# Performance work log

Hardware: AMD Instinct MI355X
Metric: run time of the kernel (lower is better)

The kernel has to match this reference:

```python
import jax, jax.numpy as jnp
import numpy as np

N_PAIR = 45  # n_agents=10 -> 10*9/2
TINY_THR = np.sqrt(np.finfo(np.float32).tiny).astype(np.float32) * N_PAIR


def setup_inputs() -> dict:
    key = jax.random.key(0)
    ks = jax.random.split(key, 8)
    bs, T, din, H = 4096, 64, 512, 64
    s = lambda fan: 1.0 / np.sqrt(fan)
    return {
        "main": jax.random.normal(ks[0], (1, bs, T, din), jnp.float32),
        "hidden_states": jnp.zeros((1, bs, 1, H), jnp.float32),
        "epsilons": jax.random.uniform(ks[1], (bs, 1), jnp.float32),
        "W_fc1": jax.random.normal(ks[2], (H, din), jnp.float32) * s(din),
        "b_fc1": jnp.zeros((H,), jnp.float32),
        "W_ih": jax.random.normal(ks[3], (3 * H, H), jnp.float32) * s(H),
        "W_hh": jax.random.normal(ks[4], (3 * H, H), jnp.float32) * s(H),
        "b_ih": jnp.zeros((3 * H,), jnp.float32),
        "b_hh": jnp.zeros((3 * H,), jnp.float32),
        "W_out": jax.random.normal(ks[5], (N_PAIR, H), jnp.float32) * s(H),
        "b_out": jnp.zeros((N_PAIR,), jnp.float32),
    }


def reference(main, hidden_states, epsilons, W_fc1, b_fc1, W_ih, W_hh, b_ih, b_hh, W_out, b_out):
    x = main[0]                       # [bs, T, din]
    h0 = hidden_states[0, :, 0, :]    # [bs, H]
    H = h0.shape[-1]

    # Encoder: fc1 + relu (time-independent, fully batched)
    enc = jax.nn.relu(jnp.einsum('bti,oi->bto', x, W_fc1) + b_fc1)  # [bs,T,H]
    # Precompute input-side GRU gates for all timesteps
    gi = jnp.einsum('bth,gh->btg', enc, W_ih) + b_ih                # [bs,T,3H]
    gi_t = jnp.transpose(gi, (1, 0, 2))                             # [T,bs,3H]

    def step(h, g_in):
        gh = h @ W_hh.T + b_hh
        i_r, i_z, i_n = jnp.split(g_in, 3, axis=-1)
        h_r, h_z, h_n = jnp.split(gh, 3, axis=-1)
        r = jax.nn.sigmoid(i_r + h_r)
        z = jax.nn.sigmoid(i_z + h_z)
        n = jnp.tanh(i_n + r * h_n)
        h_new = (1.0 - z) * n + z * h
        return h_new, h_new

    _, hs = jax.lax.scan(step, h0, gi_t)          # hs: [T,bs,H]
    hs = jnp.transpose(hs, (1, 0, 2))             # [bs,T,H]

    # Output head + custom exp-normalize with zero-sum guard
    logits = jnp.einsum('bth,oh->bto', hs, W_out) + b_out  # [bs,T,N_PAIR]
    p = jnp.exp(logits)
    p_sum = jnp.sum(p, axis=-1, keepdims=True)
    p_sum = jnp.where(p_sum <= TINY_THR, 1.0, p_sum)
    p = p / p_sum

    # Epsilon-greedy mixing (softmax exploration, not test_mode)
    eps = epsilons[:, None, :]                    # [bs,1,1]
    p = eps / N_PAIR + p * (1.0 - eps)

    x_out = p[None]                               # [1,bs,T,N_PAIR]
    h_out = hs[None]                              # [1,bs,T,H]
    return (x_out, h_out)
```

## Files before the change

### kernel.cpp

```cpp
#include <hip/hip_runtime.h>

typedef __attribute__((ext_vector_type(4))) float  f32x4;
typedef __attribute__((ext_vector_type(4))) __bf16 bf16x4;
typedef __attribute__((ext_vector_type(8))) __bf16 bf16x8;

#define MFMA16 __builtin_amdgcn_mfma_f32_16x16x32_bf16
#define TINY_THR 4.8789098e-18f
#define XOUT_N ((size_t)4096 * 64 * 45)
#define GI_LD 196

__device__ __forceinline__ void bar_lds() {
  asm volatile("s_waitcnt lgkmcnt(0)\n\ts_barrier" ::: "memory");
}

__device__ __forceinline__ int swz_off(int row, int col) {
  return row * 128 + (((col) << 1) ^ ((row & 7) << 4));
}

__device__ __forceinline__ bf16x8 read_frag(const __bf16* p, int row, int col) {
  const char* base = (const char*)p + row * 128;
  const int r7 = (row & 7) << 4;
  bf16x4 a = *(const bf16x4*)(base + (((col) << 1) ^ r7));
  bf16x4 b = *(const bf16x4*)(base + (((col + 16) << 1) ^ r7));
  bf16x8 r;
  r[0] = a[0]; r[1] = a[1]; r[2] = a[2]; r[3] = a[3];
  r[4] = b[0]; r[5] = b[1]; r[6] = b[2]; r[7] = b[3];
  return r;
}

__device__ __forceinline__ void split_bf16(float v, __bf16& h, __bf16& l) {
  h = (__bf16)v;
  l = (__bf16)(v - (float)h);
}

__global__ void k_prepW(const float* __restrict__ Wfc, __bf16* __restrict__ Wpk) {
  const int idx = blockIdx.x * 256 + threadIdx.x;
  const float v = Wfc[idx];
  __bf16 h, l; split_bf16(v, h, l);
  const int row = idx >> 9, k = idx & 511;
  const int c = k >> 6, col = k & 63;
  Wpk[(c * 2 + 0) * 4096 + row * 64 + col] = h;
  Wpk[(c * 2 + 1) * 4096 + row * 64 + col] = l;
}

__global__ __launch_bounds__(256, 4) void k_encgemm(
    const float* __restrict__ x, const __bf16* __restrict__ Wpk,
    const float* __restrict__ bfc, float* __restrict__ enc) {
  __shared__ __bf16 xs[2][64 * 64];
  __shared__ __bf16 wsm[2][64 * 64];

  const int tid  = threadIdx.x;
  const int lane = tid & 63;
  const int wv   = tid >> 6;
  const int fr   = lane & 15;
  const int q    = lane >> 4;
  const int b    = blockIdx.x;

  const int srow = tid >> 2;
  const int scol = (tid & 3) << 4;
  const float* xp = x + ((size_t)b * 64 + srow) * 512 + scol;

  f32x4 acc[4];
  #pragma unroll
  for (int nt = 0; nt < 4; ++nt) acc[nt] = (f32x4){0.f, 0.f, 0.f, 0.f};

  for (int c = 0; c < 8; ++c) {
    #pragma unroll
    for (int i = 0; i < 4; ++i) {
      f32x4 vx = *(const f32x4*)(xp + c * 64 + i * 4);
      bf16x4 xh, xl;
      #pragma unroll
      for (int j = 0; j < 4; ++j) {
        __bf16 h, l;
        split_bf16(vx[j], h, l); xh[j] = h; xl[j] = l;
      }
      const int off = swz_off(srow, scol + i * 4);
      *(bf16x4*)((char*)xs[0] + off) = xh;
      *(bf16x4*)((char*)xs[1] + off) = xl;
    }
    #pragma unroll
    for (int p = 0; p < 2; ++p) {
      const __bf16* src = Wpk + ((c * 2 + p) << 12) + srow * 64 + scol;
      bf16x8 v0 = *(const bf16x8*)(src);
      bf16x8 v1 = *(const bf16x8*)(src + 8);
      *(bf16x8*)((char*)wsm[p] + swz_off(srow, scol))     = v0;
      *(bf16x8*)((char*)wsm[p] + swz_off(srow, scol + 8)) = v1;
    }
    bar_lds();
    const int arow = wv * 16 + fr;
    bf16x8 Ah[2], Al[2];
    #pragma unroll
    for (int kk = 0; kk < 2; ++kk) {
      Ah[kk] = read_frag(xs[0], arow, kk * 32 + q * 4);
      Al[kk] = read_frag(xs[1], arow, kk * 32 + q * 4);
    }
    #pragma unroll
    for (int nt = 0; nt < 4; ++nt) {
      const int brow = nt * 16 + fr;
      #pragma unroll
      for (int kk = 0; kk < 2; ++kk) {
        bf16x8 Bh = read_frag(wsm[0], brow, kk * 32 + q * 4);
        bf16x8 Bl = read_frag(wsm[1], brow, kk * 32 + q * 4);
        acc[nt] = MFMA16(Ah[kk], Bh, acc[nt], 0, 0, 0);
        acc[nt] = MFMA16(Ah[kk], Bl, acc[nt], 0, 0, 0);
        acc[nt] = MFMA16(Al[kk], Bh, acc[nt], 0, 0, 0);
      }
    }
    bar_lds();
  }
  #pragma unroll
  for (int nt = 0; nt < 4; ++nt) {
    const int o = nt * 16 + fr;
    const float bb = bfc[o];
    #pragma unroll
    for (int e = 0; e < 4; ++e) {
      const int t = wv * 16 + q * 4 + e;
      float v = acc[nt][e] + bb;
      enc[((size_t)b * 64 + t) * 64 + o] = fmaxf(v, 0.f);
    }
  }
}

__global__ __launch_bounds__(512, 2) void k_scan(
    const float* __restrict__ enc, const float* __restrict__ h0g,
    const float* __restrict__ eps, const float* __restrict__ Wih,
    const float* __restrict__ Whh, const float* __restrict__ bih,
    const float* __restrict__ bhh, const float* __restrict__ Wout,
    const float* __restrict__ bout, float* __restrict__ xout,
    float* __restrict__ hout) {
  __shared__ __attribute__((aligned(16))) char smem[49152];
  __bf16* const wst0 = (__bf16*)smem;
  __bf16* const wst1 = (__bf16*)(smem + 24576);
  __bf16* const hp0  = (__bf16*)smem;
  __bf16* const hp1  = (__bf16*)(smem + 2048);
  __bf16* const ep0  = (__bf16*)(smem + 4096);
  __bf16* const ep1  = (__bf16*)(smem + 6144);
  float* const gi    = (float*)(smem + 8192);
  float* const lgt   = (float*)(smem + 33280);

  const int tid  = threadIdx.x;
  const int lane = tid & 63;
  const int wv   = tid >> 6;
  const int fr   = lane & 15;
  const int q    = lane >> 4;
  const int bbase = blockIdx.x * 16;
  const bool isB = (wv < 4);
  const int aw  = wv - 4;
  const int at  = tid & 255;
  const int sb  = at >> 4;
  const int sub = at & 15;
  const int so  = sub << 2;

  float hreg[4] = {0.f, 0.f, 0.f, 0.f};
  float biasNh = 0.f;
  int hcol = 0;
  float bR_ = 0.f, bZ_ = 0.f, bN_ = 0.f, boutv = 0.f, epsv = 0.f;
  if (isB) {
    hcol = wv * 16 + fr;
    biasNh = bhh[128 + hcol];
    #pragma unroll
    for (int e = 0; e < 4; ++e)
      hreg[e] = h0g[(size_t)(bbase + q * 4 + e) * 64 + hcol];
  } else {
    const int gc = aw * 16 + fr;
    bR_ = bih[gc] + bhh[gc];
    bZ_ = bih[64 + gc] + bhh[64 + gc];
    bN_ = bih[128 + gc];
    if (aw < 3 && gc < 45) boutv = bout[gc];
    epsv = eps[bbase + sb];
  }

  bf16x8 Fih[3][2][2], Fhh[3][2][2], Fout[2][2];
  for (int idx = tid; idx < 192 * 64; idx += 512) {
    __bf16 h, l; split_bf16(Wih[idx], h, l);
    const int off = swz_off(idx >> 6, idx & 63);
    *(__bf16*)((char*)wst0 + off) = h;
    *(__bf16*)((char*)wst1 + off) = l;
  }
  bar_lds();
  if (!isB) {
    #pragma unroll
    for (int t3 = 0; t3 < 3; ++t3)
      #pragma unroll
      for (int kk = 0; kk < 2; ++kk) {
        const int row = (aw + 4 * t3) * 16 + fr;
        Fih[t3][kk][0] = read_frag(wst0, row, kk * 32 + q * 4);
        Fih[t3][kk][1] = read_frag(wst1, row, kk * 32 + q * 4);
      }
  }
  bar_lds();
  for (int idx = tid; idx < 192 * 64; idx += 512) {
    __bf16 h, l; split_bf16(Whh[idx], h, l);
    const int off = swz_off(idx >> 6, idx & 63);
    *(__bf16*)((char*)wst0 + off) = h;
    *(__bf16*)((char*)wst1 + off) = l;
  }
  bar_lds();
  if (isB) {
    #pragma unroll
    for (int t3 = 0; t3 < 3; ++t3)
      #pragma unroll
      for (int kk = 0; kk < 2; ++kk) {
        const int row = (wv + 4 * t3) * 16 + fr;
        Fhh[t3][kk][0] = read_frag(wst0, row, kk * 32 + q * 4);
        Fhh[t3][kk][1] = read_frag(wst1, row, kk * 32 + q * 4);
      }
  }
  bar_lds();
  for (int idx = tid; idx < 48 * 64; idx += 512) {
    float v = (idx < 45 * 64) ? Wout[idx] : 0.f;
    __bf16 h, l; split_bf16(v, h, l);
    const int off = swz_off(idx >> 6, idx & 63);
    *(__bf16*)((char*)wst0 + off) = h;
    *(__bf16*)((char*)wst1 + off) = l;
  }
  bar_lds();
  if (!isB && aw < 3) {
    #pragma unroll
    for (int kk = 0; kk < 2; ++kk) {
      const int row = aw * 16 + fr;
      Fout[kk][0] = read_frag(wst0, row, kk * 32 + q * 4);
      Fout[kk][1] = read_frag(wst1, row, kk * 32 + q * 4);
    }
  }
  bar_lds();

  if (isB) {
    #pragma unroll
    for (int e = 0; e < 4; ++e) {
      __bf16 h, l; split_bf16(hreg[e], h, l);
      const int off = swz_off(q * 4 + e, hcol);
      *(__bf16*)((char*)hp0 + off) = h;
      *(__bf16*)((char*)hp1 + off) = l;
    }
  } else {
    f32x4 e0v = *(const f32x4*)(enc + ((size_t)(bbase + sb) * 64 + 0) * 64 + so);
    bf16x4 h4, l4;
    #pragma unroll
    for (int j = 0; j < 4; ++j) { __bf16 h, l; split_bf16(e0v[j], h, l); h4[j] = h; l4[j] = l; }
    const int off = swz_off(sb, so);
    *(bf16x4*)((char*)ep0 + off) = h4;
    *(bf16x4*)((char*)ep1 + off) = l4;
  }
  bar_lds();

  auto do_gi = [&](float* gbuf) {
    bf16x8 Eh[2], El[2];
    #pragma unroll
    for (int kk = 0; kk < 2; ++kk) {
      Eh[kk] = read_frag(ep0, fr, kk * 32 + q * 4);
      El[kk] = read_frag(ep1, fr, kk * 32 + q * 4);
    }
    f32x4 g0 = (f32x4){0.f, 0.f, 0.f, 0.f}, g1 = g0, g2 = g0;
    #pragma unroll
    for (int kk = 0; kk < 2; ++kk) {
      g0 = MFMA16(Eh[kk], Fih[0][kk][0], g0, 0, 0, 0);
      g0 = MFMA16(Eh[kk], Fih[0][kk][1], g0, 0, 0, 0);
      g0 = MFMA16(El[kk], Fih[0][kk][0], g0, 0, 0, 0);
      g1 = MFMA16(Eh[kk], Fih[1][kk][0], g1, 0, 0, 0);
      g1 = MFMA16(Eh[kk], Fih[1][kk][1], g1, 0, 0, 0);
      g1 = MFMA16(El[kk], Fih[1][kk][0], g1, 0, 0, 0);
      g2 = MFMA16(Eh[kk], Fih[2][kk][0], g2, 0, 0, 0);
      g2 = MFMA16(Eh[kk], Fih[2][kk][1], g2, 0, 0, 0);
      g2 = MFMA16(El[kk], Fih[2][kk][0], g2, 0, 0, 0);
    }
    const int gc = aw * 16 + fr;
    #pragma unroll
    for (int e = 0; e < 4; ++e) {
      const int r = (q * 4 + e) * GI_LD;
      gbuf[r + gc]       = g0[e] + bR_;
      gbuf[r + 64 + gc]  = g1[e] + bZ_;
      gbuf[r + 128 + gc] = g2[e] + bN_;
    }
  };

  f32x4 ev;
  if (!isB) {
    do_gi(gi);
    ev = *(const f32x4*)(enc + ((size_t)(bbase + sb) * 64 + 1) * 64 + so);
  }
  bar_lds();
  if (!isB) {
    bf16x4 h4, l4;
    #pragma unroll
    for (int j = 0; j < 4; ++j) { __bf16 h, l; split_bf16(ev[j], h, l); h4[j] = h; l4[j] = l; }
    const int off = swz_off(sb, so);
    *(bf16x4*)((char*)ep0 + off) = h4;
    *(bf16x4*)((char*)ep1 + off) = l4;
  }
  bar_lds();

  int cur = 0;
  for (int t = 0; t <= 64; ++t) {
    if (isB) {
      if (t < 64) {
        const float* gb = gi + cur * (16 * GI_LD);
        float giR[4], giZ[4], giN[4];
        #pragma unroll
        for (int e = 0; e < 4; ++e) {
          const int r = (q * 4 + e) * GI_LD;
          giR[e] = gb[r + hcol];
          giZ[e] = gb[r + 64 + hcol];
          giN[e] = gb[r + 128 + hcol];
        }
        bf16x8 Hh[2], Hl[2];
        #pragma unroll
        for (int kk = 0; kk < 2; ++kk) {
          Hh[kk] = read_frag(hp0, fr, kk * 32 + q * 4);
          Hl[kk] = read_frag(hp1, fr, kk * 32 + q * 4);
        }
        f32x4 aR = (f32x4){giR[0], giR[1], giR[2], giR[3]};
        f32x4 aZ = (f32x4){giZ[0], giZ[1], giZ[2], giZ[3]};
        f32x4 aN = (f32x4){0.f, 0.f, 0.f, 0.f};
        #pragma unroll
        for (int kk = 0; kk < 2; ++kk) {
          aR = MFMA16(Hh[kk], Fhh[0][kk][0], aR, 0, 0, 0);
          aR = MFMA16(Hh[kk], Fhh[0][kk][1], aR, 0, 0, 0);
          aR = MFMA16(Hl[kk], Fhh[0][kk][0], aR, 0, 0, 0);
          aZ = MFMA16(Hh[kk], Fhh[1][kk][0], aZ, 0, 0, 0);
          aZ = MFMA16(Hh[kk], Fhh[1][kk][1], aZ, 0, 0, 0);
          aZ = MFMA16(Hl[kk], Fhh[1][kk][0], aZ, 0, 0, 0);
          aN = MFMA16(Hh[kk], Fhh[2][kk][0], aN, 0, 0, 0);
          aN = MFMA16(Hh[kk], Fhh[2][kk][1], aN, 0, 0, 0);
          aN = MFMA16(Hl[kk], Fhh[2][kk][0], aN, 0, 0, 0);
        }
        #pragma unroll
        for (int e = 0; e < 4; ++e) {
          const float rr = 1.f / (1.f + __expf(-aR[e]));
          const float zz = 1.f / (1.f + __expf(-aZ[e]));
          const float npre = giN[e] + rr * (aN[e] + biasNh);
          const float nn = 2.f / (1.f + __expf(-2.f * npre)) - 1.f;
          const float hv = (1.f - zz) * nn + zz * hreg[e];
          hreg[e] = hv;
          hout[((size_t)(bbase + q * 4 + e) * 64 + t) * 64 + hcol] = hv;
        }
      }
    } else {
      if (t <= 61)
        ev = *(const f32x4*)(enc + ((size_t)(bbase + sb) * 64 + (t + 2)) * 64 + so);
      if (t <= 62) do_gi(gi + (cur ^ 1) * (16 * GI_LD));
      if (t >= 1 && aw < 3) {
        bf16x8 Hh[2], Hl[2];
        #pragma unroll
        for (int kk = 0; kk < 2; ++kk) {
          Hh[kk] = read_frag(hp0, fr, kk * 32 + q * 4);
          Hl[kk] = read_frag(hp1, fr, kk * 32 + q * 4);
        }
        f32x4 lacc = (f32x4){0.f, 0.f, 0.f, 0.f};
        #pragma unroll
        for (int kk = 0; kk < 2; ++kk) {
          lacc = MFMA16(Hh[kk], Fout[kk][0], lacc, 0, 0, 0);
          lacc = MFMA16(Hh[kk], Fout[kk][1], lacc, 0, 0, 0);
          lacc = MFMA16(Hl[kk], Fout[kk][0], lacc, 0, 0, 0);
        }
        #pragma unroll
        for (int e = 0; e < 4; ++e)
          lgt[(q * 4 + e) * 48 + aw * 16 + fr] = lacc[e] + boutv;
      }
    }
    bar_lds();
    if (isB) {
      if (t < 64) {
        #pragma unroll
        for (int e = 0; e < 4; ++e) {
          __bf16 h, l; split_bf16(hreg[e], h, l);
          const int off = swz_off(q * 4 + e, hcol);
          *(__bf16*)((char*)hp0 + off) = h;
          *(__bf16*)((char*)hp1 + off) = l;
        }
      }
    } else {
      if (t <= 61) {
        bf16x4 h4, l4;
        #pragma unroll
        for (int j = 0; j < 4; ++j) { __bf16 h, l; split_bf16(ev[j], h, l); h4[j] = h; l4[j] = l; }
        const int off = swz_off(sb, so);
        *(bf16x4*)((char*)ep0 + off) = h4;
        *(bf16x4*)((char*)ep1 + off) = l4;
      }
      if (t >= 1) {
        const float e0 = __expf(lgt[sb * 48 + sub]);
        const float e1 = (sub + 16 < 45) ? __expf(lgt[sb * 48 + sub + 16]) : 0.f;
        const float e2 = (sub + 32 < 45) ? __expf(lgt[sb * 48 + sub + 32]) : 0.f;
        float s = e0 + e1 + e2;
        s += __shfl_xor(s, 1, 16);
        s += __shfl_xor(s, 2, 16);
        s += __shfl_xor(s, 4, 16);
        s += __shfl_xor(s, 8, 16);
        if (s <= TINY_THR) s = 1.f;
        const float sc  = (1.f - epsv) / s;
        const float bse = epsv * (1.f / 45.f);
        float* orow = xout + ((size_t)(bbase + sb) * 64 + (t - 1)) * 45;
        orow[sub] = bse + e0 * sc;
        if (sub + 16 < 45) orow[sub + 16] = bse + e1 * sc;
        if (sub + 32 < 45) orow[sub + 32] = bse + e2 * sc;
      }
    }
    bar_lds();
    cur ^= 1;
  }
}

extern "C" void kernel_launch(void* const* d_in, const int* in_sizes, int n_in,
                              void* d_out, int out_size, void* d_ws, size_t ws_size,
                              hipStream_t stream) {
  (void)in_sizes; (void)n_in; (void)out_size; (void)d_ws; (void)ws_size;
  const float* x    = (const float*)d_in[0];
  const float* h0   = (const float*)d_in[1];
  const float* eps  = (const float*)d_in[2];
  const float* Wfc  = (const float*)d_in[3];
  const float* bfc  = (const float*)d_in[4];
  const float* Wih  = (const float*)d_in[5];
  const float* Whh  = (const float*)d_in[6];
  const float* bih  = (const float*)d_in[7];
  const float* bhh  = (const float*)d_in[8];
  const float* Wout = (const float*)d_in[9];
  const float* bout = (const float*)d_in[10];

  float* xout = (float*)d_out;
  float* hout = xout + XOUT_N;
  float* enc = hout;
  __bf16* Wpk = (__bf16*)d_out;

  k_prepW<<<128, 256, 0, stream>>>(Wfc, Wpk);
  k_encgemm<<<4096, 256, 0, stream>>>(x, Wpk, bfc, enc);
  k_scan<<<256, 512, 0, stream>>>(enc, h0, eps, Wih, Whh, bih, bhh, Wout, bout,
                                  xout, hout);
}
```

Before: 258.7 us.

## Async LDS staging in encoder GEMM and single-barrier double-buffered GRU scan

The encoder GEMM now copies raw fp32 x tiles and prepacked W tiles straight into double-buffered LDS with global_load_lds, overlapping the next chunk's load with the current MFMAs. The bf16 hi/lo split of x moves to after the LDS read. The scan kernel double-buffers the hidden state, encoder input and logits, which cuts each timestep to one barrier and delays the softmax one step. It also packs the GI gates into f32x4 and prefetches enc further ahead. The cost is more LDS (64KB for encgemm, lower occupancy bounds) and more complex indexing.

Result: faster. 236.5 us (-8.6%).

```diff
diff --git a/kernel.cpp b/kernel.cpp
--- a/kernel.cpp
+++ b/kernel.cpp
@@ -7,30 +7,26 @@
 #define MFMA16 __builtin_amdgcn_mfma_f32_16x16x32_bf16
 #define TINY_THR 4.8789098e-18f
 #define XOUT_N ((size_t)4096 * 64 * 45)
-#define GI_LD 196
 
 __device__ __forceinline__ void bar_lds() {
   asm volatile("s_waitcnt lgkmcnt(0)\n\ts_barrier" ::: "memory");
 }
-
-__device__ __forceinline__ int swz_off(int row, int col) {
-  return row * 128 + (((col) << 1) ^ ((row & 7) << 4));
-}
-
-__device__ __forceinline__ bf16x8 read_frag(const __bf16* p, int row, int col) {
-  const char* base = (const char*)p + row * 128;
-  const int r7 = (row & 7) << 4;
-  bf16x4 a = *(const bf16x4*)(base + (((col) << 1) ^ r7));
-  bf16x4 b = *(const bf16x4*)(base + (((col + 16) << 1) ^ r7));
-  bf16x8 r;
-  r[0] = a[0]; r[1] = a[1]; r[2] = a[2]; r[3] = a[3];
-  r[4] = b[0]; r[5] = b[1]; r[6] = b[2]; r[7] = b[3];
-  return r;
-}
-
 __device__ __forceinline__ void split_bf16(float v, __bf16& h, __bf16& l) {
-  h = (__bf16)v;
-  l = (__bf16)(v - (float)h);
+  h = (__bf16)v; l = (__bf16)(v - (float)h);
+}
+__device__ __forceinline__ void gll16(const void* g, void* l) {
+  __builtin_amdgcn_global_load_lds(
+      (const __attribute__((address_space(1))) void*)g,
+      (__attribute__((address_space(3))) void*)l, 16, 0, 0);
+}
+
+__device__ __forceinline__ int pk_off(int row, int col) {
+  const int kk = col >> 5, rem = col & 31;
+  const int half = rem >> 4, qq = (rem >> 2) & 3, j = rem & 3;
+  return row * 128 + ((((kk << 2) | qq) ^ (row & 7)) << 4) + half * 8 + j * 2;
+}
+__device__ __forceinline__ bf16x8 frag_pk(const char* base, int row, int kk, int qq) {
+  return *(const bf16x8*)(base + row * 128 + ((((kk << 2) | qq) ^ (row & 7)) << 4));
 }
 
 __global__ void k_prepW(const float* __restrict__ Wfc, __bf16* __restrict__ Wpk) {
@@ -38,17 +34,19 @@
   const float v = Wfc[idx];
   __bf16 h, l; split_bf16(v, h, l);
   const int row = idx >> 9, k = idx & 511;
-  const int c = k >> 6, col = k & 63;
-  Wpk[(c * 2 + 0) * 4096 + row * 64 + col] = h;
-  Wpk[(c * 2 + 1) * 4096 + row * 64 + col] = l;
-}
-
-__global__ __launch_bounds__(256, 4) void k_encgemm(
+  const int c = k >> 6, kl = k & 63;
+  const int kk = kl >> 5, rem = kl & 31;
+  const int half = rem >> 4, q = (rem >> 2) & 3, j = rem & 3;
+  const int blk = ((kk << 2) | q) ^ (row & 7);
+  const int pos = c * 8192 + row * 64 + blk * 8 + half * 4 + j;
+  Wpk[pos] = h;
+  Wpk[pos + 4096] = l;
+}
+
+__global__ __launch_bounds__(256, 2) void k_encgemm(
     const float* __restrict__ x, const __bf16* __restrict__ Wpk,
     const float* __restrict__ bfc, float* __restrict__ enc) {
-  __shared__ __bf16 xs[2][64 * 64];
-  __shared__ __bf16 wsm[2][64 * 64];
-
+  __shared__ __attribute__((aligned(16))) char sm[65536];
   const int tid  = threadIdx.x;
   const int lane = tid & 63;
   const int wv   = tid >> 6;
@@ -56,57 +54,67 @@
   const int q    = lane >> 4;
   const int b    = blockIdx.x;
 
-  const int srow = tid >> 2;
-  const int scol = (tid & 3) << 4;
-  const float* xp = x + ((size_t)b * 64 + srow) * 512 + scol;
+  auto stage = [&](int c, int buf) {
+    char* xbase = sm + buf * 16384;
+    char* wbase = sm + 32768 + buf * 16384;
+    #pragma unroll
+    for (int i = 0; i < 4; ++i) {
+      const int B   = wv * 256 + i * 64 + lane;
+      const int row = B >> 4, blk = B & 15;
+      const int bp  = blk ^ (row & 15);
+      const int colb = ((bp >> 3) << 5) | ((bp & 1) << 4) | (((bp >> 1) & 3) << 2);
+      const float* src = x + ((size_t)b * 64 + row) * 512 + c * 64 + colb;
+      gll16(src, xbase + wv * 4096 + i * 1024);
+    }
+    #pragma unroll
+    for (int i = 0; i < 4; ++i) {
+      const __bf16* srcw = Wpk + c * 8192 + wv * 2048 + i * 512 + lane * 8;
+      gll16(srcw, wbase + wv * 4096 + i * 1024);
+    }
+  };
 
   f32x4 acc[4];
   #pragma unroll
   for (int nt = 0; nt < 4; ++nt) acc[nt] = (f32x4){0.f, 0.f, 0.f, 0.f};
 
+  stage(0, 0);
+  int buf = 0;
   for (int c = 0; c < 8; ++c) {
-    #pragma unroll
-    for (int i = 0; i < 4; ++i) {
-      f32x4 vx = *(const f32x4*)(xp + c * 64 + i * 4);
-      bf16x4 xh, xl;
+    if (c < 7) {
+      stage(c + 1, buf ^ 1);
+      asm volatile("s_waitcnt vmcnt(8)\n\ts_barrier" ::: "memory");
+    } else {
+      asm volatile("s_waitcnt vmcnt(0)\n\ts_barrier" ::: "memory");
+    }
+    const char* xbase = sm + buf * 16384;
+    const char* wbase = sm + 32768 + buf * 16384;
+    const int arow = wv * 16 + fr;
+    bf16x8 Ah[2], Al[2];
+    #pragma unroll
+    for (int kk = 0; kk < 2; ++kk) {
+      f32x4 u0 = *(const f32x4*)(xbase + arow * 256 + (((kk * 8 + q * 2 + 0) ^ (arow & 15)) << 4));
+      f32x4 u1 = *(const f32x4*)(xbase + arow * 256 + (((kk * 8 + q * 2 + 1) ^ (arow & 15)) << 4));
       #pragma unroll
       for (int j = 0; j < 4; ++j) {
         __bf16 h, l;
-        split_bf16(vx[j], h, l); xh[j] = h; xl[j] = l;
-      }
-      const int off = swz_off(srow, scol + i * 4);
-      *(bf16x4*)((char*)xs[0] + off) = xh;
-      *(bf16x4*)((char*)xs[1] + off) = xl;
-    }
-    #pragma unroll
-    for (int p = 0; p < 2; ++p) {
-      const __bf16* src = Wpk + ((c * 2 + p) << 12) + srow * 64 + scol;
-      bf16x8 v0 = *(const bf16x8*)(src);
-      bf16x8 v1 = *(const bf16x8*)(src + 8);
-      *(bf16x8*)((char*)wsm[p] + swz_off(srow, scol))     = v0;
-      *(bf16x8*)((char*)wsm[p] + swz_off(srow, scol + 8)) = v1;
-    }
-    bar_lds();
-    const int arow = wv * 16 + fr;
-    bf16x8 Ah[2], Al[2];
-    #pragma unroll
-    for (int kk = 0; kk < 2; ++kk) {
-      Ah[kk] = read_frag(xs[0], arow, kk * 32 + q * 4);
-      Al[kk] = read_frag(xs[1], arow, kk * 32 + q * 4);
+        split_bf16(u0[j], h, l); Ah[kk][j] = h;     Al[kk][j] = l;
+        split_bf16(u1[j], h, l); Ah[kk][4 + j] = h; Al[kk][4 + j] = l;
+      }
     }
     #pragma unroll
     for (int nt = 0; nt < 4; ++nt) {
       const int brow = nt * 16 + fr;
       #pragma unroll
       for (int kk = 0; kk < 2; ++kk) {
-        bf16x8 Bh = read_frag(wsm[0], brow, kk * 32 + q * 4);
-        bf16x8 Bl = read_frag(wsm[1], brow, kk * 32 + q * 4);
+        bf16x8 Bh = frag_pk(wbase, brow, kk, q);
+        bf16x8 Bl = frag_pk(wbase + 8192, brow, kk, q);
         acc[nt] = MFMA16(Ah[kk], Bh, acc[nt], 0, 0, 0);
         acc[nt] = MFMA16(Ah[kk], Bl, acc[nt], 0, 0, 0);
         acc[nt] = MFMA16(Al[kk], Bh, acc[nt], 0, 0, 0);
       }
     }
     bar_lds();
+    buf ^= 1;
   }
   #pragma unroll
   for (int nt = 0; nt < 4; ++nt) {
@@ -121,22 +129,16 @@
   }
 }
 
-__global__ __launch_bounds__(512, 2) void k_scan(
+__global__ __launch_bounds__(512, 1) void k_scan(
     const float* __restrict__ enc, const float* __restrict__ h0g,
     const float* __restrict__ eps, const float* __restrict__ Wih,
     const float* __restrict__ Whh, const float* __restrict__ bih,
     const float* __restrict__ bhh, const float* __restrict__ Wout,
     const float* __restrict__ bout, float* __restrict__ xout,
     float* __restrict__ hout) {
-  __shared__ __attribute__((aligned(16))) char smem[49152];
-  __bf16* const wst0 = (__bf16*)smem;
-  __bf16* const wst1 = (__bf16*)(smem + 24576);
-  __bf16* const hp0  = (__bf16*)smem;
-  __bf16* const hp1  = (__bf16*)(smem + 2048);
-  __bf16* const ep0  = (__bf16*)(smem + 4096);
-  __bf16* const ep1  = (__bf16*)(smem + 6144);
-  float* const gi    = (float*)(smem + 8192);
-  float* const lgt   = (float*)(smem + 33280);
+  __shared__ __attribute__((aligned(16))) char sm[55808];
+  char* const wst0 = sm;
+  char* const wst1 = sm + 24576;
 
   const int tid  = threadIdx.x;
   const int lane = tid & 63;
@@ -173,9 +175,9 @@
   bf16x8 Fih[3][2][2], Fhh[3][2][2], Fout[2][2];
   for (int idx = tid; idx < 192 * 64; idx += 512) {
     __bf16 h, l; split_bf16(Wih[idx], h, l);
-    const int off = swz_off(idx >> 6, idx & 63);
-    *(__bf16*)((char*)wst0 + off) = h;
-    *(__bf16*)((char*)wst1 + off) = l;
+    const int off = pk_off(idx >> 6, idx & 63);
+    *(__bf16*)(wst0 + off) = h;
+    *(__bf16*)(wst1 + off) = l;
   }
   bar_lds();
   if (!isB) {
@@ -184,16 +186,16 @@
       #pragma unroll
       for (int kk = 0; kk < 2; ++kk) {
         const int row = (aw + 4 * t3) * 16 + fr;
-        Fih[t3][kk][0] = read_frag(wst0, row, kk * 32 + q * 4);
-        Fih[t3][kk][1] = read_frag(wst1, row, kk * 32 + q * 4);
+        Fih[t3][kk][0] = frag_pk(wst0, row, kk, q);
+        Fih[t3][kk][1] = frag_pk(wst1, row, kk, q);
       }
   }
   bar_lds();
   for (int idx = tid; idx < 192 * 64; idx += 512) {
     __bf16 h, l; split_bf16(Whh[idx], h, l);
-    const int off = swz_off(idx >> 6, idx & 63);
-    *(__bf16*)((char*)wst0 + off) = h;
-    *(__bf16*)((char*)wst1 + off) = l;
+    const int off = pk_off(idx >> 6, idx & 63);
+    *(__bf16*)(wst0 + off) = h;
+    *(__bf16*)(wst1 + off) = l;
   }
   bar_lds();
   if (isB) {
@@ -202,54 +204,46 @@
       #pragma unroll
       for (int kk = 0; kk < 2; ++kk) {
         const int row = (wv + 4 * t3) * 16 + fr;
-        Fhh[t3][kk][0] = read_frag(wst0, row, kk * 32 + q * 4);
-        Fhh[t3][kk][1] = read_frag(wst1, row, kk * 32 + q * 4);
+        Fhh[t3][kk][0] = frag_pk(wst0, row, kk, q);
+        Fhh[t3][kk][1] = frag_pk(wst1, row, kk, q);
       }
   }
   bar_lds();
   for (int idx = tid; idx < 48 * 64; idx += 512) {
     float v = (idx < 45 * 64) ? Wout[idx] : 0.f;
     __bf16 h, l; split_bf16(v, h, l);
-    const int off = swz_off(idx >> 6, idx & 63);
-    *(__bf16*)((char*)wst0 + off) = h;
-    *(__bf16*)((char*)wst1 + off) = l;
+    const int off = pk_off(idx >> 6, idx & 63);
+    *(__bf16*)(wst0 + off) = h;
+    *(__bf16*)(wst1 + off) = l;
   }
   bar_lds();
   if (!isB && aw < 3) {
     #pragma unroll
     for (int kk = 0; kk < 2; ++kk) {
       const int row = aw * 16 + fr;
-      Fout[kk][0] = read_frag(wst0, row, kk * 32 + q * 4);
-      Fout[kk][1] = read_frag(wst1, row, kk * 32 + q * 4);
-    }
-  }
-  bar_lds();
-
-  if (isB) {
-    #pragma unroll
-    for (int e = 0; e < 4; ++e) {
-      __bf16 h, l; split_bf16(hreg[e], h, l);
-      const int off = swz_off(q * 4 + e, hcol);
-      *(__bf16*)((char*)hp0 + off) = h;
-      *(__bf16*)((char*)hp1 + off) = l;
-    }
-  } else {
-    f32x4 e0v = *(const f32x4*)(enc + ((size_t)(bbase + sb) * 64 + 0) * 64 + so);
+      Fout[kk][0] = frag_pk(wst0, row, kk, q);
+      Fout[kk][1] = frag_pk(wst1, row, kk, q);
+    }
+  }
+  bar_lds();
+
+  auto put_epd = [&](int dst, const f32x4& ev) {
     bf16x4 h4, l4;
     #pragma unroll
-    for (int j = 0; j < 4; ++j) { __bf16 h, l; split_bf16(e0v[j], h, l); h4[j] = h; l4[j] = l; }
-    const int off = swz_off(sb, so);
-    *(bf16x4*)((char*)ep0 + off) = h4;
-    *(bf16x4*)((char*)ep1 + off) = l4;
-  }
-  bar_lds();
-
-  auto do_gi = [&](float* gbuf) {
+    for (int j = 0; j < 4; ++j) { __bf16 h, l; split_bf16(ev[j], h, l); h4[j] = h; l4[j] = l; }
+    char* p0 = sm + 8192 + dst * 4096;
+    const int off = pk_off(sb, so);
+    *(bf16x4*)(p0 + off) = h4;
+    *(bf16x4*)(p0 + 2048 + off) = l4;
+  };
+  auto do_gi = [&](int src, int dst) {
+    const char* e0c = sm + 8192 + src * 4096;
+    const char* e1c = e0c + 2048;
     bf16x8 Eh[2], El[2];
     #pragma unroll
     for (int kk = 0; kk < 2; ++kk) {
-      Eh[kk] = read_frag(ep0, fr, kk * 32 + q * 4);
-      El[kk] = read_frag(ep1, fr, kk * 32 + q * 4);
+      Eh[kk] = frag_pk(e0c, fr, kk, q);
+      El[kk] = frag_pk(e1c, fr, kk, q);
     }
     f32x4 g0 = (f32x4){0.f, 0.f, 0.f, 0.f}, g1 = g0, g2 = g0;
     #pragma unroll
@@ -264,53 +258,58 @@
       g2 = MFMA16(Eh[kk], Fih[2][kk][1], g2, 0, 0, 0);
       g2 = MFMA16(El[kk], Fih[2][kk][0], g2, 0, 0, 0);
     }
+    float* gw = (float*)(sm + 16384 + dst * 16640);
     const int gc = aw * 16 + fr;
     #pragma unroll
     for (int e = 0; e < 4; ++e) {
-      const int r = (q * 4 + e) * GI_LD;
-      gbuf[r + gc]       = g0[e] + bR_;
-      gbuf[r + 64 + gc]  = g1[e] + bZ_;
-      gbuf[r + 128 + gc] = g2[e] + bN_;
+      f32x4 o = (f32x4){g0[e] + bR_, g1[e] + bZ_, g2[e] + bN_, 0.f};
+      *(f32x4*)(gw + (q * 4 + e) * 260 + gc * 4) = o;
     }
   };
 
-  f32x4 ev;
+  f32x4 evA, evB;
   if (!isB) {
-    do_gi(gi);
-    ev = *(const f32x4*)(enc + ((size_t)(bbase + sb) * 64 + 1) * 64 + so);
-  }
-  bar_lds();
-  if (!isB) {
-    bf16x4 h4, l4;
-    #pragma unroll
-    for (int j = 0; j < 4; ++j) { __bf16 h, l; split_bf16(ev[j], h, l); h4[j] = h; l4[j] = l; }
-    const int off = swz_off(sb, so);
-    *(bf16x4*)((char*)ep0 + off) = h4;
-    *(bf16x4*)((char*)ep1 + off) = l4;
-  }
-  bar_lds();
-
-  int cur = 0;
-  for (int t = 0; t <= 64; ++t) {
+    const float* eb = enc + (size_t)(bbase + sb) * 64 * 64 + so;
+    f32x4 e0v = *(const f32x4*)(eb);
+    f32x4 e1v = *(const f32x4*)(eb + 64);
+    evA = *(const f32x4*)(eb + 2 * 64);
+    evB = *(const f32x4*)(eb + 3 * 64);
+    put_epd(1, e0v);
+    bar_lds();
+    do_gi(1, 0);
+    put_epd(0, e1v);
+  } else {
+    char* h0b = sm;
+    char* h1b = sm + 2048;
+    #pragma unroll
+    for (int e = 0; e < 4; ++e) {
+      __bf16 h, l; split_bf16(hreg[e], h, l);
+      const int off = pk_off(q * 4 + e, hcol);
+      *(__bf16*)(h0b + off) = h;
+      *(__bf16*)(h1b + off) = l;
+    }
+    bar_lds();
+  }
+  bar_lds();
+
+  auto body = [&](int t, int cur, f32x4& evC) {
     if (isB) {
-      if (t < 64) {
-        const float* gb = gi + cur * (16 * GI_LD);
-        float giR[4], giZ[4], giN[4];
-        #pragma unroll
-        for (int e = 0; e < 4; ++e) {
-          const int r = (q * 4 + e) * GI_LD;
-          giR[e] = gb[r + hcol];
-          giZ[e] = gb[r + 64 + hcol];
-          giN[e] = gb[r + 128 + hcol];
+      if (t <= 63) {
+        const float* gr = (const float*)(sm + 16384 + cur * 16640);
+        f32x4 gv[4];
+        #pragma unroll
+        for (int e = 0; e < 4; ++e)
+          gv[e] = *(const f32x4*)(gr + (q * 4 + e) * 260 + hcol * 4);
+        const char* hp0c = sm + cur * 4096;
+        const char* hp1c = hp0c + 2048;
+        bf16x8 Hh[2], Hl[2];
+        #pragma unroll
+        for (int kk = 0; kk < 2; ++kk) {
+          Hh[kk] = frag_pk(hp0c, fr, kk, q);
+          Hl[kk] = frag_pk(hp1c, fr, kk, q);
         }
-        bf16x8 Hh[2], Hl[2];
-        #pragma unroll
-        for (int kk = 0; kk < 2; ++kk) {
-          Hh[kk] = read_frag(hp0, fr, kk * 32 + q * 4);
-          Hl[kk] = read_frag(hp1, fr, kk * 32 + q * 4);
-        }
-        f32x4 aR = (f32x4){giR[0], giR[1], giR[2], giR[3]};
-        f32x4 aZ = (f32x4){giZ[0], giZ[1], giZ[2], giZ[3]};
+        f32x4 aR = (f32x4){gv[0][0], gv[1][0], gv[2][0], gv[3][0]};
+        f32x4 aZ = (f32x4){gv[0][1], gv[1][1], gv[2][1], gv[3][1]};
         f32x4 aN = (f32x4){0.f, 0.f, 0.f, 0.f};
         #pragma unroll
         for (int kk = 0; kk < 2; ++kk) {
@@ -324,27 +323,33 @@
           aN = MFMA16(Hh[kk], Fhh[2][kk][1], aN, 0, 0, 0);
           aN = MFMA16(Hl[kk], Fhh[2][kk][0], aN, 0, 0, 0);
         }
+        char* n0 = sm + (cur ^ 1) * 4096;
+        char* n1 = n0 + 2048;
         #pragma unroll
         for (int e = 0; e < 4; ++e) {
           const float rr = 1.f / (1.f + __expf(-aR[e]));
           const float zz = 1.f / (1.f + __expf(-aZ[e]));
-          const float npre = giN[e] + rr * (aN[e] + biasNh);
+          const float npre = gv[e][2] + rr * (aN[e] + biasNh);
           const float nn = 2.f / (1.f + __expf(-2.f * npre)) - 1.f;
           const float hv = (1.f - zz) * nn + zz * hreg[e];
           hreg[e] = hv;
           hout[((size_t)(bbase + q * 4 + e) * 64 + t) * 64 + hcol] = hv;
+          __bf16 h, l; split_bf16(hv, h, l);
+          const int off = pk_off(q * 4 + e, hcol);
+          *(__bf16*)(n0 + off) = h;
+          *(__bf16*)(n1 + off) = l;
         }
       }
     } else {
-      if (t <= 61)
-        ev = *(const f32x4*)(enc + ((size_t)(bbase + sb) * 64 + (t + 2)) * 64 + so);
-      if (t <= 62) do_gi(gi + (cur ^ 1) * (16 * GI_LD));
-      if (t >= 1 && aw < 3) {
+      if (t <= 62) do_gi(cur, cur ^ 1);
+      if (t >= 1 && t <= 64 && aw < 3) {
+        const char* hp0c = sm + cur * 4096;
+        const char* hp1c = hp0c + 2048;
         bf16x8 Hh[2], Hl[2];
         #pragma unroll
         for (int kk = 0; kk < 2; ++kk) {
-          Hh[kk] = read_frag(hp0, fr, kk * 32 + q * 4);
-          Hl[kk] = read_frag(hp1, fr, kk * 32 + q * 4);
+          Hh[kk] = frag_pk(hp0c, fr, kk, q);
+          Hl[kk] = frag_pk(hp1c, fr, kk, q);
         }
         f32x4 lacc = (f32x4){0.f, 0.f, 0.f, 0.f};
         #pragma unroll
@@ -353,35 +358,19 @@
           lacc = MFMA16(Hh[kk], Fout[kk][1], lacc, 0, 0, 0);
           lacc = MFMA16(Hl[kk], Fout[kk][0], lacc, 0, 0, 0);
         }
+        float* lg = (float*)(sm + 49664 + (cur ^ 1) * 3072);
         #pragma unroll
         for (int e = 0; e < 4; ++e)
-          lgt[(q * 4 + e) * 48 + aw * 16 + fr] = lacc[e] + boutv;
-      }
-    }
-    bar_lds();
-    if (isB) {
-      if (t < 64) {
-        #pragma unroll
-        for (int e = 0; e < 4; ++e) {
-          __bf16 h, l; split_bf16(hreg[e], h, l);
-          const int off = swz_off(q * 4 + e, hcol);
-          *(__bf16*)((char*)hp0 + off) = h;
-          *(__bf16*)((char*)hp1 + off) = l;
-        }
-      }
-    } else {
-      if (t <= 61) {
-        bf16x4 h4, l4;
-        #pragma unroll
-        for (int j = 0; j < 4; ++j) { __bf16 h, l; split_bf16(ev[j], h, l); h4[j] = h; l4[j] = l; }
-        const int off = swz_off(sb, so);
-        *(bf16x4*)((char*)ep0 + off) = h4;
-        *(bf16x4*)((char*)ep1 + off) = l4;
-      }
-      if (t >= 1) {
-        const float e0 = __expf(lgt[sb * 48 + sub]);
-        const float e1 = (sub + 16 < 45) ? __expf(lgt[sb * 48 + sub + 16]) : 0.f;
-        const float e2 = (sub + 32 < 45) ? __expf(lgt[sb * 48 + sub + 32]) : 0.f;
+          lg[(q * 4 + e) * 48 + aw * 16 + fr] = lacc[e] + boutv;
+      }
+      if (t <= 61) put_epd(cur ^ 1, evC);
+      if (t <= 59)
+        evC = *(const f32x4*)(enc + ((size_t)(bbase + sb) * 64 + (t + 4)) * 64 + so);
+      if (t >= 2) {
+        const float* lg = (const float*)(sm + 49664 + cur * 3072);
+        const float e0 = __expf(lg[sb * 48 + sub]);
+        const float e1 = (sub + 16 < 45) ? __expf(lg[sb * 48 + sub + 16]) : 0.f;
+        const float e2 = (sub + 32 < 45) ? __expf(lg[sb * 48 + sub + 32]) : 0.f;
         float s = e0 + e1 + e2;
         s += __shfl_xor(s, 1, 16);
         s += __shfl_xor(s, 2, 16);
@@ -390,14 +379,18 @@
         if (s <= TINY_THR) s = 1.f;
         const float sc  = (1.f - epsv) / s;
         const float bse = epsv * (1.f / 45.f);
-        float* orow = xout + ((size_t)(bbase + sb) * 64 + (t - 1)) * 45;
+        float* orow = xout + ((size_t)(bbase + sb) * 64 + (t - 2)) * 45;
         orow[sub] = bse + e0 * sc;
         if (sub + 16 < 45) orow[sub + 16] = bse + e1 * sc;
         if (sub + 32 < 45) orow[sub + 32] = bse + e2 * sc;
       }
     }
     bar_lds();
-    cur ^= 1;
+  };
+
+  for (int t2 = 0; t2 < 66; t2 += 2) {
+    body(t2, 0, evA);
+    body(t2 + 1, 1, evB);
   }
 }
 
```
